# Optimization experiments

Measured on AMD Instinct MI355X. Metric: run time of the kernel, lower is better.

Reference implementation:

```python
import jax, jax.numpy as jnp
import numpy as np

N, DEG, D, D2, B, NEG = 65536, 16, 64, 128, 1024, 10
EPS = 1e-12  # F.normalize eps


def setup_inputs() -> dict:
    key = jax.random.key(0)
    ks = jax.random.split(key, 9)
    s1 = 1.0 / np.sqrt(2 * D)
    s2 = 1.0 / np.sqrt(2 * D)
    return {
        "feat_data": jax.random.normal(ks[0], (N, D), jnp.float32),
        "adj": jax.random.randint(ks[1], (N, DEG), 0, N),
        "inputs1": jax.random.randint(ks[2], (B,), 0, N),
        "inputs2": jax.random.randint(ks[3], (B,), 0, N),
        "neg": jax.random.randint(ks[4], (NEG,), 0, N),
        "W1": jax.random.uniform(ks[5], (D, 2 * D), jnp.float32, -s1, s1),
        "b1": jax.random.uniform(ks[6], (D,), jnp.float32, -s1, s1),
        "W2": jax.random.uniform(ks[7], (D2, 2 * D), jnp.float32, -s2, s2),
        "b2": jax.random.uniform(ks[8], (D2,), jnp.float32, -s2, s2),
    }


def reference(feat_data, adj, inputs1, inputs2, neg, W1, b1, W2, b2):
    # Hop-1: per-node neighbor feature sum (gather + reduce), concat self, linear1, tanh.
    # Computed for all nodes (superset of the union the original builds; same values).
    sum1 = feat_data[adj].sum(axis=1)                      # [N, D] gather-heavy
    h1 = jnp.tanh(jnp.concatenate([feat_data, sum1], axis=-1) @ W1.T + b1)  # [N, D]

    def emb(nodes):
        # Hop-2: sum hop-1 embeddings of neighbors, concat raw self features, linear2.
        sum2 = h1[adj[nodes]].sum(axis=1)                  # [b, D]
        out = jnp.concatenate([feat_data[nodes], sum2], axis=-1) @ W2.T + b2  # [b, D2]
        nrm = jnp.maximum(jnp.linalg.norm(out, axis=1, keepdims=True), EPS)
        return out / nrm

    return emb(inputs1), emb(inputs2), emb(neg)
```

## Files before the change

### kernel.cpp

```cpp
#include <hip/hip_runtime.h>
#include <math.h>

#define NN   65536
#define DEGC 16
#define DD   64
#define DD2  128
#define BB   1024
#define NEGC 10
#define NROWS (2 * BB + NEGC)
#define NEDGE (NROWS * DEGC)

__device__ __forceinline__ float tanh_fast(float x) {
    float t = __expf(2.0f * x);
    return 1.0f - 2.0f * __builtin_amdgcn_rcpf(t + 1.0f);
}

__device__ __forceinline__ unsigned short f2bf(float v) {
    unsigned int x = __float_as_uint(v);
    x += 0x7FFFu + ((x >> 16) & 1u);
    return (unsigned short)(x >> 16);
}
__device__ __forceinline__ float bf2f(unsigned short u) {
    return __uint_as_float(((unsigned int)u) << 16);
}

__global__ __launch_bounds__(256) void pq_gemm_kernel(
    const float* __restrict__ feat, const float* __restrict__ W1,
    const float* __restrict__ b1,
    unsigned short* __restrict__ Pb, unsigned short* __restrict__ Qb) {

    __shared__ float4 qa[1024];
    __shared__ float4 qb[1024];
    int tid = threadIdx.x;
    {
        int j = tid & 63, g = tid >> 6;
        #pragma unroll
        for (int t = 0; t < 4; ++t) {
            int i4 = g * 4 + t;
            qa[(i4 << 6) | j] = *(const float4*)(W1 + j * DD2 + i4 * 4);
            qb[(i4 << 6) | j] = *(const float4*)(W1 + j * DD2 + DD + i4 * 4);
        }
    }
    __syncthreads();

    int lane = tid & 63;
    int w = tid >> 6;
    int nbase = __builtin_amdgcn_readfirstlane((blockIdx.x * 4 + w) * 4);

    const float* f0 = feat + (size_t)(nbase + 0) * DD;
    const float* f1 = feat + (size_t)(nbase + 1) * DD;
    const float* f2 = feat + (size_t)(nbase + 2) * DD;
    const float* f3 = feat + (size_t)(nbase + 3) * DD;

    float bias = b1[lane];
    float pa0 = bias, pa1 = bias, pa2 = bias, pa3 = bias;
    float qv0 = 0.f, qv1 = 0.f, qv2 = 0.f, qv3 = 0.f;
    #pragma unroll
    for (int i4 = 0; i4 < 16; ++i4) {
        float4 wa = qa[(i4 << 6) | lane];
        float4 wb = qb[(i4 << 6) | lane];
        float4 c0 = *(const float4*)(f0 + i4 * 4);
        float4 c1 = *(const float4*)(f1 + i4 * 4);
        float4 c2 = *(const float4*)(f2 + i4 * 4);
        float4 c3 = *(const float4*)(f3 + i4 * 4);
        pa0 += c0.x * wa.x + c0.y * wa.y + c0.z * wa.z + c0.w * wa.w;
        pa1 += c1.x * wa.x + c1.y * wa.y + c1.z * wa.z + c1.w * wa.w;
        pa2 += c2.x * wa.x + c2.y * wa.y + c2.z * wa.z + c2.w * wa.w;
        pa3 += c3.x * wa.x + c3.y * wa.y + c3.z * wa.z + c3.w * wa.w;
        qv0 += c0.x * wb.x + c0.y * wb.y + c0.z * wb.z + c0.w * wb.w;
        qv1 += c1.x * wb.x + c1.y * wb.y + c1.z * wb.z + c1.w * wb.w;
        qv2 += c2.x * wb.x + c2.y * wb.y + c2.z * wb.z + c2.w * wb.w;
        qv3 += c3.x * wb.x + c3.y * wb.y + c3.z * wb.z + c3.w * wb.w;
    }
    Pb[(size_t)(nbase + 0) * DD + lane] = f2bf(pa0);
    Pb[(size_t)(nbase + 1) * DD + lane] = f2bf(pa1);
    Pb[(size_t)(nbase + 2) * DD + lane] = f2bf(pa2);
    Pb[(size_t)(nbase + 3) * DD + lane] = f2bf(pa3);
    Qb[(size_t)(nbase + 0) * DD + lane] = f2bf(qv0);
    Qb[(size_t)(nbase + 1) * DD + lane] = f2bf(qv1);
    Qb[(size_t)(nbase + 2) * DD + lane] = f2bf(qv2);
    Qb[(size_t)(nbase + 3) * DD + lane] = f2bf(qv3);
}

__global__ __launch_bounds__(256) void edge_kernel(
    const int* __restrict__ adj,
    const int* __restrict__ in1, const int* __restrict__ in2,
    const int* __restrict__ neg,
    const unsigned short* __restrict__ Pb, const unsigned short* __restrict__ Qb,
    float* __restrict__ h1) {

    int tid = threadIdx.x;
    int lane = tid & 63;
    int g = lane >> 4;
    int q = lane & 15;
    int wid = blockIdx.x * 4 + (tid >> 6);
    int ebase = wid * 4;
    int r = ebase >> 4;
    int kbase = ebase & 15;

    int node = (r < BB) ? in1[r] : (r < 2 * BB ? in2[r - BB] : neg[r - 2 * BB]);
    node = __builtin_amdgcn_readfirstlane(node);
    const int* arow = adj + node * DEGC + kbase;
    int n0 = __builtin_amdgcn_readfirstlane(arow[0]);
    int n1 = __builtin_amdgcn_readfirstlane(arow[1]);
    int n2 = __builtin_amdgcn_readfirstlane(arow[2]);
    int n3 = __builtin_amdgcn_readfirstlane(arow[3]);
    int n_g = (g == 0) ? n0 : (g == 1) ? n1 : (g == 2) ? n2 : n3;

    int nbr = adj[(size_t)n_g * DEGC + q];

    float a0, a1, a2, a3;
    {
        unsigned long long v = *(const unsigned long long*)(Pb + (size_t)n_g * DD + q * 4);
        a0 = bf2f((unsigned short)(v));
        a1 = bf2f((unsigned short)(v >> 16));
        a2 = bf2f((unsigned short)(v >> 32));
        a3 = bf2f((unsigned short)(v >> 48));
    }

    #pragma unroll
    for (int i = 0; i < DEGC; ++i) {
        int row = __shfl(nbr, g * 16 + i, 64);
        unsigned long long v = *(const unsigned long long*)(Qb + (size_t)row * DD + q * 4);
        a0 += bf2f((unsigned short)(v));
        a1 += bf2f((unsigned short)(v >> 16));
        a2 += bf2f((unsigned short)(v >> 32));
        a3 += bf2f((unsigned short)(v >> 48));
    }

    float4 o;
    o.x = tanh_fast(a0);
    o.y = tanh_fast(a1);
    o.z = tanh_fast(a2);
    o.w = tanh_fast(a3);
    *(float4*)(h1 + (size_t)(ebase + g) * DD + q * 4) = o;
}

__global__ __launch_bounds__(256) void hop2_fused(
    const float* __restrict__ feat, const float* __restrict__ h1,
    const int* __restrict__ in1, const int* __restrict__ in2,
    const int* __restrict__ neg,
    const float* __restrict__ W2, const float* __restrict__ b2,
    float* __restrict__ out) {

    __shared__ float4 q2[4096];
    __shared__ float4 cs4[8][16];

    int tid = threadIdx.x;
    {
        int j = tid & 127, g0 = tid >> 7;
        #pragma unroll
        for (int g = 0; g < 16; ++g) {
            int i4 = g0 * 16 + g;
            q2[(i4 << 7) | j] = *(const float4*)(W2 + j * DD2 + (i4 << 2));
        }
    }

    int lane = tid & 63;
    int w = tid >> 6;
    int r0 = blockIdx.x * 8 + w * 2;
    int r1 = r0 + 1;
    bool a0 = r0 < NROWS, a1 = r1 < NROWS;

    #pragma unroll
    for (int m = 0; m < 2; ++m) {
        int r = r0 + m;
        if (r < NROWS) {
            const float* base = h1 + (size_t)r * DEGC * DD;
            float s = 0.f;
            #pragma unroll
            for (int k = 0; k < DEGC; ++k)
                s += base[k * DD + lane];
            ((float*)&cs4[w * 2 + m][0])[lane] = s;
        }
    }
    __syncthreads();

    int node0 = a0 ? ((r0 < BB) ? in1[r0] : (r0 < 2 * BB ? in2[r0 - BB] : neg[r0 - 2 * BB])) : 0;
    int node1 = a1 ? ((r1 < BB) ? in1[r1] : (r1 < 2 * BB ? in2[r1 - BB] : neg[r1 - 2 * BB])) : node0;
    node0 = __builtin_amdgcn_readfirstlane(node0);
    node1 = __builtin_amdgcn_readfirstlane(node1);
    const float* cf0 = feat + (size_t)node0 * DD;
    const float* cf1 = feat + (size_t)node1 * DD;

    float A0 = b2[lane], B0 = b2[DD + lane];
    float A1 = A0, B1 = B0;

    #pragma unroll
    for (int i4 = 0; i4 < 16; ++i4) {
        float4 wA = q2[(i4 << 7) | lane];
        float4 wB = q2[(i4 << 7) | (64 + lane)];
        float4 c0 = *(const float4*)(cf0 + (i4 << 2));
        float4 c1 = *(const float4*)(cf1 + (i4 << 2));
        A0 += c0.x * wA.x + c0.y * wA.y + c0.z * wA.z + c0.w * wA.w;
        B0 += c0.x * wB.x + c0.y * wB.y + c0.z * wB.z + c0.w * wB.w;
        A1 += c1.x * wA.x + c1.y * wA.y + c1.z * wA.z + c1.w * wA.w;
        B1 += c1.x * wB.x + c1.y * wB.y + c1.z * wB.z + c1.w * wB.w;
    }
    #pragma unroll
    for (int i4 = 0; i4 < 16; ++i4) {
        float4 wA = q2[((16 + i4) << 7) | lane];
        float4 wB = q2[((16 + i4) << 7) | (64 + lane)];
        float4 c0 = cs4[w * 2 + 0][i4];
        float4 c1 = cs4[w * 2 + 1][i4];
        A0 += c0.x * wA.x + c0.y * wA.y + c0.z * wA.z + c0.w * wA.w;
        B0 += c0.x * wB.x + c0.y * wB.y + c0.z * wB.z + c0.w * wB.w;
        A1 += c1.x * wA.x + c1.y * wA.y + c1.z * wA.z + c1.w * wA.w;
        B1 += c1.x * wB.x + c1.y * wB.y + c1.z * wB.z + c1.w * wB.w;
    }

    if (a0) {
        float ss = A0 * A0 + B0 * B0;
        #pragma unroll
        for (int off = 32; off > 0; off >>= 1) ss += __shfl_xor(ss, off, 64);
        float inv = 1.0f / fmaxf(sqrtf(ss), 1e-12f);
        out[r0 * DD2 + lane]      = A0 * inv;
        out[r0 * DD2 + DD + lane] = B0 * inv;
    }
    if (a1) {
        float ss = A1 * A1 + B1 * B1;
        #pragma unroll
        for (int off = 32; off > 0; off >>= 1) ss += __shfl_xor(ss, off, 64);
        float inv = 1.0f / fmaxf(sqrtf(ss), 1e-12f);
        out[r1 * DD2 + lane]      = A1 * inv;
        out[r1 * DD2 + DD + lane] = B1 * inv;
    }
}

extern "C" void kernel_launch(void* const* d_in, const int* in_sizes, int n_in,
                              void* d_out, int out_size, void* d_ws, size_t ws_size,
                              hipStream_t stream) {
    const float* feat = (const float*)d_in[0];
    const int*   adj  = (const int*)d_in[1];
    const int*   in1  = (const int*)d_in[2];
    const int*   in2  = (const int*)d_in[3];
    const int*   neg  = (const int*)d_in[4];
    const float* W1   = (const float*)d_in[5];
    const float* b1   = (const float*)d_in[6];
    const float* W2   = (const float*)d_in[7];
    const float* b2   = (const float*)d_in[8];
    float* out = (float*)d_out;

    char* p = (char*)d_ws;
    unsigned short* Pb = (unsigned short*)p;   size_t off = (size_t)NN * DD * sizeof(unsigned short);
    unsigned short* Qb = (unsigned short*)(p + off); off += (size_t)NN * DD * sizeof(unsigned short);
    float* h1 = (float*)(p + off);

    pq_gemm_kernel<<<NN / 16, 256, 0, stream>>>(feat, W1, b1, Pb, Qb);
    edge_kernel<<<NEDGE / 16, 256, 0, stream>>>(adj, in1, in2, neg, Pb, Qb, h1);
    hop2_fused<<<(NROWS + 7) / 8, 256, 0, stream>>>(
        feat, h1, in1, in2, neg, W2, b2, out);
}
```

Measured before the change: 59.33 us.

## Reduce hop-2 neighbor sums inside the edge kernel instead of storing per-edge h1

The edge kernel now processes one output row per block. It reduces the 16 tanh-ed hop-1 embeddings in registers and shared memory and writes a single 64-float sum per row, instead of writing 16 per-edge h1 rows. The final GEMV kernel reads that precomputed sum, so it no longer reloads and reduces 16 h1 rows per output. This removes roughly 2 MB of intermediate writes and reads, at the cost of an extra __syncthreads and cross-lane shuffles in the edge stage.

```diff
diff --git a/kernel.cpp b/kernel.cpp
--- a/kernel.cpp
+++ b/kernel.cpp
@@ -82,25 +82,25 @@
     Qb[(size_t)(nbase + 3) * DD + lane] = f2bf(qv3);
 }
 
-__global__ __launch_bounds__(256) void edge_kernel(
+__global__ __launch_bounds__(256) void row_kernel(
     const int* __restrict__ adj,
     const int* __restrict__ in1, const int* __restrict__ in2,
     const int* __restrict__ neg,
     const unsigned short* __restrict__ Pb, const unsigned short* __restrict__ Qb,
-    float* __restrict__ h1) {
+    float* __restrict__ csum2) {
+
+    __shared__ float cs[4][DD];
 
     int tid = threadIdx.x;
     int lane = tid & 63;
+    int w = tid >> 6;
     int g = lane >> 4;
     int q = lane & 15;
-    int wid = blockIdx.x * 4 + (tid >> 6);
-    int ebase = wid * 4;
-    int r = ebase >> 4;
-    int kbase = ebase & 15;
+    int r = blockIdx.x;
 
     int node = (r < BB) ? in1[r] : (r < 2 * BB ? in2[r - BB] : neg[r - 2 * BB]);
     node = __builtin_amdgcn_readfirstlane(node);
-    const int* arow = adj + node * DEGC + kbase;
+    const int* arow = adj + node * DEGC + w * 4;
     int n0 = __builtin_amdgcn_readfirstlane(arow[0]);
     int n1 = __builtin_amdgcn_readfirstlane(arow[1]);
     int n2 = __builtin_amdgcn_readfirstlane(arow[2]);
@@ -117,7 +117,6 @@
         a2 = bf2f((unsigned short)(v >> 32));
         a3 = bf2f((unsigned short)(v >> 48));
     }
-
     #pragma unroll
     for (int i = 0; i < DEGC; ++i) {
         int row = __shfl(nbr, g * 16 + i, 64);
@@ -127,25 +126,35 @@
         a2 += bf2f((unsigned short)(v >> 32));
         a3 += bf2f((unsigned short)(v >> 48));
     }
-
-    float4 o;
-    o.x = tanh_fast(a0);
-    o.y = tanh_fast(a1);
-    o.z = tanh_fast(a2);
-    o.w = tanh_fast(a3);
-    *(float4*)(h1 + (size_t)(ebase + g) * DD + q * 4) = o;
-}
-
-__global__ __launch_bounds__(256) void hop2_fused(
-    const float* __restrict__ feat, const float* __restrict__ h1,
+    a0 = tanh_fast(a0); a1 = tanh_fast(a1);
+    a2 = tanh_fast(a2); a3 = tanh_fast(a3);
+
+    a0 += __shfl_xor(a0, 16, 64); a0 += __shfl_xor(a0, 32, 64);
+    a1 += __shfl_xor(a1, 16, 64); a1 += __shfl_xor(a1, 32, 64);
+    a2 += __shfl_xor(a2, 16, 64); a2 += __shfl_xor(a2, 32, 64);
+    a3 += __shfl_xor(a3, 16, 64); a3 += __shfl_xor(a3, 32, 64);
+
+    if (g == 0) {
+        cs[w][q * 4 + 0] = a0;
+        cs[w][q * 4 + 1] = a1;
+        cs[w][q * 4 + 2] = a2;
+        cs[w][q * 4 + 3] = a3;
+    }
+    __syncthreads();
+    if (w == 0) {
+        float s = cs[0][lane] + cs[1][lane] + cs[2][lane] + cs[3][lane];
+        csum2[(size_t)r * DD + lane] = s;
+    }
+}
+
+__global__ __launch_bounds__(256) void gemv2_kernel(
+    const float* __restrict__ feat,
     const int* __restrict__ in1, const int* __restrict__ in2,
     const int* __restrict__ neg,
-    const float* __restrict__ W2, const float* __restrict__ b2,
-    float* __restrict__ out) {
+    const float* __restrict__ csum2, const float* __restrict__ W2,
+    const float* __restrict__ b2, float* __restrict__ out) {
 
     __shared__ float4 q2[4096];
-    __shared__ float4 cs4[8][16];
-
     int tid = threadIdx.x;
     {
         int j = tid & 127, g0 = tid >> 7;
@@ -155,33 +164,22 @@
             q2[(i4 << 7) | j] = *(const float4*)(W2 + j * DD2 + (i4 << 2));
         }
     }
+    __syncthreads();
 
     int lane = tid & 63;
-    int w = tid >> 6;
-    int r0 = blockIdx.x * 8 + w * 2;
-    int r1 = r0 + 1;
+    int wv = blockIdx.x * 4 + (tid >> 6);
+    int r0 = wv * 2, r1 = wv * 2 + 1;
     bool a0 = r0 < NROWS, a1 = r1 < NROWS;
-
-    #pragma unroll
-    for (int m = 0; m < 2; ++m) {
-        int r = r0 + m;
-        if (r < NROWS) {
-            const float* base = h1 + (size_t)r * DEGC * DD;
-            float s = 0.f;
-            #pragma unroll
-            for (int k = 0; k < DEGC; ++k)
-                s += base[k * DD + lane];
-            ((float*)&cs4[w * 2 + m][0])[lane] = s;
-        }
-    }
-    __syncthreads();
-
-    int node0 = a0 ? ((r0 < BB) ? in1[r0] : (r0 < 2 * BB ? in2[r0 - BB] : neg[r0 - 2 * BB])) : 0;
+    if (!a0) return;
+
+    int node0 = (r0 < BB) ? in1[r0] : (r0 < 2 * BB ? in2[r0 - BB] : neg[r0 - 2 * BB]);
     int node1 = a1 ? ((r1 < BB) ? in1[r1] : (r1 < 2 * BB ? in2[r1 - BB] : neg[r1 - 2 * BB])) : node0;
     node0 = __builtin_amdgcn_readfirstlane(node0);
     node1 = __builtin_amdgcn_readfirstlane(node1);
     const float* cf0 = feat + (size_t)node0 * DD;
     const float* cf1 = feat + (size_t)node1 * DD;
+    const float* cs0 = csum2 + (size_t)r0 * DD;
+    const float* cs1 = csum2 + (size_t)(a1 ? r1 : r0) * DD;
 
     float A0 = b2[lane], B0 = b2[DD + lane];
     float A1 = A0, B1 = B0;
@@ -201,29 +199,29 @@
     for (int i4 = 0; i4 < 16; ++i4) {
         float4 wA = q2[((16 + i4) << 7) | lane];
         float4 wB = q2[((16 + i4) << 7) | (64 + lane)];
-        float4 c0 = cs4[w * 2 + 0][i4];
-        float4 c1 = cs4[w * 2 + 1][i4];
+        float4 c0 = *(const float4*)(cs0 + (i4 << 2));
+        float4 c1 = *(const float4*)(cs1 + (i4 << 2));
         A0 += c0.x * wA.x + c0.y * wA.y + c0.z * wA.z + c0.w * wA.w;
         B0 += c0.x * wB.x + c0.y * wB.y + c0.z * wB.z + c0.w * wB.w;
         A1 += c1.x * wA.x + c1.y * wA.y + c1.z * wA.z + c1.w * wA.w;
         B1 += c1.x * wB.x + c1.y * wB.y + c1.z * wB.z + c1.w * wB.w;
     }
 
-    if (a0) {
+    {
         float ss = A0 * A0 + B0 * B0;
         #pragma unroll
         for (int off = 32; off > 0; off >>= 1) ss += __shfl_xor(ss, off, 64);
         float inv = 1.0f / fmaxf(sqrtf(ss), 1e-12f);
-        out[r0 * DD2 + lane]      = A0 * inv;
-        out[r0 * DD2 + DD + lane] = B0 * inv;
+        out[(size_t)r0 * DD2 + lane]      = A0 * inv;
+        out[(size_t)r0 * DD2 + DD + lane] = B0 * inv;
     }
     if (a1) {
         float ss = A1 * A1 + B1 * B1;
         #pragma unroll
         for (int off = 32; off > 0; off >>= 1) ss += __shfl_xor(ss, off, 64);
         float inv = 1.0f / fmaxf(sqrtf(ss), 1e-12f);
-        out[r1 * DD2 + lane]      = A1 * inv;
-        out[r1 * DD2 + DD + lane] = B1 * inv;
+        out[(size_t)r1 * DD2 + lane]      = A1 * inv;
+        out[(size_t)r1 * DD2 + DD + lane] = B1 * inv;
     }
 }
 
@@ -242,12 +240,14 @@
     float* out = (float*)d_out;
 
     char* p = (char*)d_ws;
-    unsigned short* Pb = (unsigned short*)p;   size_t off = (size_t)NN * DD * sizeof(unsigned short);
-    unsigned short* Qb = (unsigned short*)(p + off); off += (size_t)NN * DD * sizeof(unsigned short);
-    float* h1 = (float*)(p + off);
+    unsigned short* Pb = (unsigned short*)p;
+    size_t off = (size_t)NN * DD * sizeof(unsigned short);
+    unsigned short* Qb = (unsigned short*)(p + off);
+    off += (size_t)NN * DD * sizeof(unsigned short);
+    float* csum2 = (float*)(p + off);
 
     pq_gemm_kernel<<<NN / 16, 256, 0, stream>>>(feat, W1, b1, Pb, Qb);
-    edge_kernel<<<NEDGE / 16, 256, 0, stream>>>(adj, in1, in2, neg, Pb, Qb, h1);
-    hop2_fused<<<(NROWS + 7) / 8, 256, 0, stream>>>(
-        feat, h1, in1, in2, neg, W2, b2, out);
-}
+    row_kernel<<<NROWS, 256, 0, stream>>>(adj, in1, in2, neg, Pb, Qb, csum2);
+    gemv2_kernel<<<(NROWS + 7) / 8, 256, 0, stream>>>(
+        feat, in1, in2, neg, csum2, W2, b2, out);
+}
```

After: 62.56 us. +5.4%, slower.
